# Kernel optimization log

Hardware: AMD Instinct MI355X
Metric: run time of the kernel (lower is better)

## Reference

```python
import jax, jax.numpy as jnp
import numpy as np

TOK = 256        # flattened batch*seq tokens (decode-style, memory-bound)
IN_F = 4096
OUT_F = 4096
N_OUTLIER = 32


def quantize_rowwise(x):
    """Symmetric rowwise int8 quantization: scale = rowwise absmax."""
    scale = jnp.max(jnp.abs(x), axis=-1)                      # [rows]
    safe = jnp.maximum(scale, 1e-8)
    q = jnp.clip(jnp.round(x / safe[:, None] * 127.0), -127.0, 127.0)
    return q, scale


def setup_inputs() -> dict:
    key = jax.random.key(0)
    k1, k2, k3, k4, k5 = jax.random.split(key, 5)
    x = jax.random.normal(k1, (TOK, IN_F), jnp.float32)
    weight_int8 = jax.random.randint(k2, (OUT_F, IN_F), -127, 128, jnp.int32)
    weight_scales = jax.random.uniform(k3, (OUT_F,), jnp.float32, minval=0.5, maxval=2.0)
    # spread unique outlier column indices across in_features
    outlier_indices = jnp.arange(N_OUTLIER, dtype=jnp.int32) * (IN_F // N_OUTLIER)
    outlier_weights = jax.random.normal(k4, (OUT_F, N_OUTLIER), jnp.float32) * 0.02
    bias = jax.random.normal(k5, (OUT_F,), jnp.float32) * 0.01
    # from_linear zeros outlier columns of the int8 weight before quantization
    weight_int8 = weight_int8.at[:, outlier_indices].set(0)
    return {"x": x, "weight_int8": weight_int8, "weight_scales": weight_scales,
            "outlier_indices": outlier_indices, "outlier_weights": outlier_weights,
            "bias": bias}


def reference(x, weight_int8, weight_scales, outlier_indices, outlier_weights, bias):
    # _forward_mixed: outlier columns handled in fp, rest quantize->dequant int8.
    # Selecting the non-outlier columns is equivalent to zeroing the outlier
    # columns (the dropped weight columns contribute 0 to the GEMM, and the
    # rowwise absmax scale is unaffected since |0| = 0). This keeps shapes
    # static and jit-friendly while computing identical math.
    in_f = x.shape[-1]
    mask = jnp.ones((in_f,), dtype=bool).at[outlier_indices].set(False)

    x_main = x * mask                                         # [T, in]
    xq, xs = quantize_rowwise(x_main)                         # int8-valued fp, [T]
    x_fp = xq * (xs[:, None] / 127.0)                         # dequantized activations

    w_fp = (weight_int8 * mask).astype(jnp.float32) * (weight_scales[:, None] / 127.0)  # [out, in]
    out_main = x_fp @ w_fp.T                                  # [T, out]

    x_outlier = x[:, outlier_indices]                         # [T, n_out]
    out_outlier = x_outlier @ outlier_weights.T               # [T, out]

    return out_main + out_outlier + bias
```

## Files before the change

### kernel.cpp

```cpp
#include <hip/hip_runtime.h>
#include <stdint.h>

#define TOK 256
#define IN_F 4096
#define OUT_F 4096
#define N_OUT 32

#define BN 16
#define MACRO_K 512
#define NMACRO (IN_F / MACRO_K)
#define KSTEPS (MACRO_K / 64)

typedef int v4i __attribute__((ext_vector_type(4)));

__global__ __launch_bounds__(256) void oal_quant(
    const float* __restrict__ x, const int* __restrict__ oidx,
    int8_t* __restrict__ xq, float* __restrict__ xs, float* __restrict__ xo)
{
    const int row = blockIdx.x;
    const int tid = threadIdx.x;
    __shared__ unsigned char flags[IN_F];
    __shared__ float wmax[4];
    __shared__ float s_scale;

    *reinterpret_cast<uint4*>(&flags[tid * 16]) = make_uint4(0u, 0u, 0u, 0u);
    __syncthreads();
    if (tid < N_OUT) flags[oidx[tid]] = 1;
    __syncthreads();

    const float* xr = x + (size_t)row * IN_F;
    float4 v[4];
    const float4* xp = reinterpret_cast<const float4*>(xr + tid * 16);
    #pragma unroll
    for (int i = 0; i < 4; ++i) v[i] = xp[i];

    uint4 f = *reinterpret_cast<const uint4*>(&flags[tid * 16]);
    unsigned int fw[4] = { f.x, f.y, f.z, f.w };
    float vals[16];
    #pragma unroll
    for (int i = 0; i < 4; ++i) {
        vals[i*4+0] = ((fw[i]      ) & 255u) ? 0.0f : v[i].x;
        vals[i*4+1] = ((fw[i] >>  8) & 255u) ? 0.0f : v[i].y;
        vals[i*4+2] = ((fw[i] >> 16) & 255u) ? 0.0f : v[i].z;
        vals[i*4+3] = ((fw[i] >> 24) & 255u) ? 0.0f : v[i].w;
    }

    float m = 0.0f;
    #pragma unroll
    for (int i = 0; i < 16; ++i) m = fmaxf(m, fabsf(vals[i]));
    #pragma unroll
    for (int off = 32; off > 0; off >>= 1) m = fmaxf(m, __shfl_xor(m, off, 64));
    const int lane = tid & 63, wid = tid >> 6;
    if (lane == 0) wmax[wid] = m;
    __syncthreads();
    if (tid == 0) {
        float s = fmaxf(fmaxf(wmax[0], wmax[1]), fmaxf(wmax[2], wmax[3]));
        s_scale = s;
        xs[row] = s;
    }
    __syncthreads();
    const float safe = fmaxf(s_scale, 1e-8f);

    int q[16];
    #pragma unroll
    for (int i = 0; i < 16; ++i) {
        float t = vals[i] / safe * 127.0f;
        t = fminf(127.0f, fmaxf(-127.0f, rintf(t)));
        q[i] = (int)t;
    }
    uint4 packed;
    unsigned int* pw = &packed.x;
    #pragma unroll
    for (int i = 0; i < 4; ++i)
        pw[i] = (unsigned)(q[i*4] & 255) | ((unsigned)(q[i*4+1] & 255) << 8)
              | ((unsigned)(q[i*4+2] & 255) << 16) | ((unsigned)(q[i*4+3] & 255) << 24);
    *reinterpret_cast<uint4*>(xq + (size_t)row * IN_F + tid * 16) = packed;

    if (tid < N_OUT) xo[row * N_OUT + tid] = xr[oidx[tid]];
}

__global__ __launch_bounds__(512, 2) void oal_gemm(
    const int8_t* __restrict__ xq, const int* __restrict__ w,
    const float* __restrict__ xs, const float* __restrict__ wscale,
    const float* __restrict__ ow, const float* __restrict__ bias,
    const float* __restrict__ xo, float* __restrict__ out)
{
    const int bn = blockIdx.x;
    const int tid = threadIdx.x;
    const int lane = tid & 63;
    const int wv = tid >> 6;

    __shared__ __align__(16) signed char Bs[2][BN][528];
    __shared__ __align__(16) float XO[TOK][N_OUT];

    {
        const float4* src = reinterpret_cast<const float4*>(xo);
        float4* dst = reinterpret_cast<float4*>(&XO[0][0]);
        #pragma unroll
        for (int i = 0; i < 4; ++i) dst[tid * 4 + i] = src[tid * 4 + i];
    }

    const int sr = tid >> 5;
    const int sc = tid & 31;
    const int* wbase = w + (size_t)(bn * BN + sr) * IN_F + sc * 16;

    int4 wr_[4];
    auto load_regs = [&](int mm) {
        const int4* p = reinterpret_cast<const int4*>(wbase + mm * MACRO_K);
        #pragma unroll
        for (int i = 0; i < 4; ++i) wr_[i] = p[i];
    };
    auto pack_store = [&](int buf) {
        int p[4];
        #pragma unroll
        for (int i = 0; i < 4; ++i) {
            int4 a = wr_[i];
            p[i] = (a.x & 255) | ((a.y & 255) << 8) | ((a.z & 255) << 16) | ((a.w & 255) << 24);
        }
        *reinterpret_cast<int4*>(&Bs[buf][sr][sc * 16]) = make_int4(p[0], p[1], p[2], p[3]);
    };

    const int mrow = wv * 32;
    const int koff_lane = (lane >> 4) * 16;
    const int8_t* a0p = xq + (size_t)(mrow + (lane & 15)) * IN_F + koff_lane;
    const int8_t* a1p = a0p + 16 * IN_F;

    v4i acc0 = {0, 0, 0, 0}, acc1 = {0, 0, 0, 0};

    load_regs(0);
    pack_store(0);
    load_regs(1);
    __syncthreads();

    #pragma unroll
    for (int mm = 0; mm < NMACRO; ++mm) {
        const int cur = mm & 1;
        #pragma unroll
        for (int kk = 0; kk < KSTEPS; ++kk) {
            const int kg = mm * MACRO_K + kk * 64;
            v4i av0 = *reinterpret_cast<const v4i*>(a0p + kg);
            v4i av1 = *reinterpret_cast<const v4i*>(a1p + kg);
            v4i bv  = *reinterpret_cast<const v4i*>(&Bs[cur][lane & 15][kk * 64 + koff_lane]);
            acc0 = __builtin_amdgcn_mfma_i32_16x16x64_i8(av0, bv, acc0, 0, 0, 0);
            acc1 = __builtin_amdgcn_mfma_i32_16x16x64_i8(av1, bv, acc1, 0, 0, 0);
        }
        if (mm < NMACRO - 1) {
            pack_store(cur ^ 1);
            if (mm < NMACRO - 2) load_regs(mm + 2);
            __syncthreads();
        }
    }

    const int ocol = bn * BN + (lane & 15);
    const float wsc = wscale[ocol] * (1.0f / 16129.0f);
    const float bo  = bias[ocol];
    float4 owr[8];
    const float4* owp = reinterpret_cast<const float4*>(ow + (size_t)ocol * N_OUT);
    #pragma unroll
    for (int i = 0; i < 8; ++i) owr[i] = owp[i];

    const int rbase = (lane >> 4) * 4;
    #pragma unroll
    for (int mt = 0; mt < 2; ++mt) {
        v4i a = mt ? acc1 : acc0;
        #pragma unroll
        for (int r = 0; r < 4; ++r) {
            const int t = mrow + mt * 16 + rbase + r;
            const float* xr2 = &XO[t][0];
            float dot = 0.0f;
            #pragma unroll
            for (int j = 0; j < 8; ++j) {
                float4 o4 = owr[j];
                dot += xr2[j*4+0]*o4.x + xr2[j*4+1]*o4.y + xr2[j*4+2]*o4.z + xr2[j*4+3]*o4.w;
            }
            out[(size_t)t * OUT_F + ocol] = (float)a[r] * (xs[t] * wsc) + bo + dot;
        }
    }
}

extern "C" void kernel_launch(void* const* d_in, const int* in_sizes, int n_in,
                              void* d_out, int out_size, void* d_ws, size_t ws_size,
                              hipStream_t stream) {
    const float* x      = (const float*)d_in[0];
    const int*   w      = (const int*)  d_in[1];
    const float* wscale = (const float*)d_in[2];
    const int*   oidx   = (const int*)  d_in[3];
    const float* ow     = (const float*)d_in[4];
    const float* bias   = (const float*)d_in[5];
    float* out = (float*)d_out;

    int8_t* xq = (int8_t*)d_ws;
    float*  xs = (float*)((char*)d_ws + (size_t)TOK * IN_F);
    float*  xo = (float*)((char*)d_ws + (size_t)TOK * IN_F + 1024);

    oal_quant<<<TOK, 256, 0, stream>>>(x, oidx, xq, xs, xo);
    oal_gemm<<<OUT_F / BN, 512, 0, stream>>>(xq, w, xs, wscale, ow, bias, xo, out);
}
```

Baseline: 138.8 us.

## Deepen weight prefetch to two stages and register-pipeline activation loads

The GEMM now keeps two register sets of int32 weights in flight, prefetching macro-tile mm+3 while packing mm+1, so the global-load latency is hidden across more compute. Activation fragments for the MFMA are held in a four-deep register ring and loaded four k-steps ahead instead of just before use. Launch bounds drop from two blocks per SM to one to give the extra registers room, and the quant kernel issues its x loads before the shared-flag setup barriers. The trade is higher register pressure and lower occupancy in exchange for more memory-level parallelism.

```diff
diff --git a/kernel.cpp b/kernel.cpp
--- a/kernel.cpp
+++ b/kernel.cpp
@@ -7,9 +7,10 @@
 #define N_OUT 32
 
 #define BN 16
-#define MACRO_K 512
-#define NMACRO (IN_F / MACRO_K)
-#define KSTEPS (MACRO_K / 64)
+#define KSTEP 64
+#define NK 64
+#define KPM 8
+#define NMACRO 8
 
 typedef int v4i __attribute__((ext_vector_type(4)));
 
@@ -23,16 +24,16 @@
     __shared__ float wmax[4];
     __shared__ float s_scale;
 
-    *reinterpret_cast<uint4*>(&flags[tid * 16]) = make_uint4(0u, 0u, 0u, 0u);
-    __syncthreads();
-    if (tid < N_OUT) flags[oidx[tid]] = 1;
-    __syncthreads();
-
     const float* xr = x + (size_t)row * IN_F;
     float4 v[4];
     const float4* xp = reinterpret_cast<const float4*>(xr + tid * 16);
     #pragma unroll
     for (int i = 0; i < 4; ++i) v[i] = xp[i];
+
+    *reinterpret_cast<uint4*>(&flags[tid * 16]) = make_uint4(0u, 0u, 0u, 0u);
+    __syncthreads();
+    if (tid < N_OUT) flags[oidx[tid]] = 1;
+    __syncthreads();
 
     uint4 f = *reinterpret_cast<const uint4*>(&flags[tid * 16]);
     unsigned int fw[4] = { f.x, f.y, f.z, f.w };
@@ -79,7 +80,7 @@
     if (tid < N_OUT) xo[row * N_OUT + tid] = xr[oidx[tid]];
 }
 
-__global__ __launch_bounds__(512, 2) void oal_gemm(
+__global__ __launch_bounds__(512, 1) void oal_gemm(
     const int8_t* __restrict__ xq, const int* __restrict__ w,
     const float* __restrict__ xs, const float* __restrict__ wscale,
     const float* __restrict__ ow, const float* __restrict__ bias,
@@ -104,52 +105,63 @@
     const int sc = tid & 31;
     const int* wbase = w + (size_t)(bn * BN + sr) * IN_F + sc * 16;
 
-    int4 wr_[4];
-    auto load_regs = [&](int mm) {
-        const int4* p = reinterpret_cast<const int4*>(wbase + mm * MACRO_K);
+    int4 wa[4], wb[4];
+
+#define LOADW(R, mm) { const int4* p_ = reinterpret_cast<const int4*>(wbase + (mm) * (KPM * KSTEP)); \
+    R[0] = p_[0]; R[1] = p_[1]; R[2] = p_[2]; R[3] = p_[3]; }
+
+#define PACKW(R, buf) { int pk0_ = (R[0].x & 255) | ((R[0].y & 255) << 8) | ((R[0].z & 255) << 16) | ((R[0].w & 255) << 24); \
+    int pk1_ = (R[1].x & 255) | ((R[1].y & 255) << 8) | ((R[1].z & 255) << 16) | ((R[1].w & 255) << 24); \
+    int pk2_ = (R[2].x & 255) | ((R[2].y & 255) << 8) | ((R[2].z & 255) << 16) | ((R[2].w & 255) << 24); \
+    int pk3_ = (R[3].x & 255) | ((R[3].y & 255) << 8) | ((R[3].z & 255) << 16) | ((R[3].w & 255) << 24); \
+    *reinterpret_cast<int4*>(&Bs[buf][sr][sc * 16]) = make_int4(pk0_, pk1_, pk2_, pk3_); }
+
+    const int mrow = wv * 32;
+    const int koff = (lane >> 4) * 16;
+    const int8_t* a0p = xq + (size_t)(mrow + (lane & 15)) * IN_F + koff;
+    const int8_t* a1p = a0p + 16 * IN_F;
+
+    v4i acc0 = {0, 0, 0, 0}, acc1 = {0, 0, 0, 0};
+    v4i ar0[4], ar1[4];
+
+    LOADW(wa, 0);
+    LOADW(wb, 1);
+    #pragma unroll
+    for (int i = 0; i < 4; ++i) {
+        ar0[i] = *reinterpret_cast<const v4i*>(a0p + i * KSTEP);
+        ar1[i] = *reinterpret_cast<const v4i*>(a1p + i * KSTEP);
+    }
+    PACKW(wa, 0);
+    LOADW(wa, 2);
+    __syncthreads();
+
+    #pragma unroll
+    for (int mm = 0; mm < NMACRO; ++mm) {
         #pragma unroll
-        for (int i = 0; i < 4; ++i) wr_[i] = p[i];
-    };
-    auto pack_store = [&](int buf) {
-        int p[4];
-        #pragma unroll
-        for (int i = 0; i < 4; ++i) {
-            int4 a = wr_[i];
-            p[i] = (a.x & 255) | ((a.y & 255) << 8) | ((a.z & 255) << 16) | ((a.w & 255) << 24);
-        }
-        *reinterpret_cast<int4*>(&Bs[buf][sr][sc * 16]) = make_int4(p[0], p[1], p[2], p[3]);
-    };
-
-    const int mrow = wv * 32;
-    const int koff_lane = (lane >> 4) * 16;
-    const int8_t* a0p = xq + (size_t)(mrow + (lane & 15)) * IN_F + koff_lane;
-    const int8_t* a1p = a0p + 16 * IN_F;
-
-    v4i acc0 = {0, 0, 0, 0}, acc1 = {0, 0, 0, 0};
-
-    load_regs(0);
-    pack_store(0);
-    load_regs(1);
-    __syncthreads();
-
-    #pragma unroll
-    for (int mm = 0; mm < NMACRO; ++mm) {
-        const int cur = mm & 1;
-        #pragma unroll
-        for (int kk = 0; kk < KSTEPS; ++kk) {
-            const int kg = mm * MACRO_K + kk * 64;
-            v4i av0 = *reinterpret_cast<const v4i*>(a0p + kg);
-            v4i av1 = *reinterpret_cast<const v4i*>(a1p + kg);
-            v4i bv  = *reinterpret_cast<const v4i*>(&Bs[cur][lane & 15][kk * 64 + koff_lane]);
-            acc0 = __builtin_amdgcn_mfma_i32_16x16x64_i8(av0, bv, acc0, 0, 0, 0);
-            acc1 = __builtin_amdgcn_mfma_i32_16x16x64_i8(av1, bv, acc1, 0, 0, 0);
+        for (int kk = 0; kk < KPM; ++kk) {
+            const int ks = mm * KPM + kk;
+            v4i bv = *reinterpret_cast<const v4i*>(&Bs[mm & 1][lane & 15][kk * KSTEP + koff]);
+            acc0 = __builtin_amdgcn_mfma_i32_16x16x64_i8(ar0[ks & 3], bv, acc0, 0, 0, 0);
+            acc1 = __builtin_amdgcn_mfma_i32_16x16x64_i8(ar1[ks & 3], bv, acc1, 0, 0, 0);
+            if (ks + 4 < NK) {
+                ar0[ks & 3] = *reinterpret_cast<const v4i*>(a0p + (ks + 4) * KSTEP);
+                ar1[ks & 3] = *reinterpret_cast<const v4i*>(a1p + (ks + 4) * KSTEP);
+            }
         }
         if (mm < NMACRO - 1) {
-            pack_store(cur ^ 1);
-            if (mm < NMACRO - 2) load_regs(mm + 2);
+            if ((mm & 1) == 0) {
+                PACKW(wb, (mm + 1) & 1);
+                if (mm + 3 < NMACRO) LOADW(wb, mm + 3);
+            } else {
+                PACKW(wa, (mm + 1) & 1);
+                if (mm + 3 < NMACRO) LOADW(wa, mm + 3);
+            }
             __syncthreads();
         }
     }
+
+#undef LOADW
+#undef PACKW
 
     const int ocol = bn * BN + (lane & 15);
     const float wsc = wscale[ocol] * (1.0f / 16129.0f);
```

After: 137.2 us. Within noise of the previous version (-1.1%).

## Stage activations into LDS via async global_load_lds with triple-buffered K pipeline

Applied to the files above, without the earlier changes.

The quant kernel now writes the int8 activations in a K-tiled, XOR-swizzled layout, so each 64-wide K slice of all tokens is contiguous. The GEMM uses global_load_lds to stream those tiles directly into a three-stage LDS ring. Weights are loaded as small per-step chunks and packed into a swizzled LDS buffer, with manual vmcnt/lgkmcnt waits and raw barriers. The outlier activations are now read from global memory instead of being staged in LDS. This aims to cut redundant global activation loads and overlap memory with MFMA, at the cost of a barrier every 64-K step and lower occupancy (launch bounds set to 1 block per CU).

```diff
diff --git a/kernel.cpp b/kernel.cpp
--- a/kernel.cpp
+++ b/kernel.cpp
@@ -5,17 +5,25 @@
 #define IN_F 4096
 #define OUT_F 4096
 #define N_OUT 32
-
 #define BN 16
-#define MACRO_K 512
-#define NMACRO (IN_F / MACRO_K)
-#define KSTEPS (MACRO_K / 64)
+#define TILE_A 16384
 
 typedef int v4i __attribute__((ext_vector_type(4)));
+
+typedef const __attribute__((address_space(1))) void cg_void;
+typedef __attribute__((address_space(3))) void lds_void;
+
+__device__ __forceinline__ void gll16(const void* g, void* l) {
+    __builtin_amdgcn_global_load_lds((cg_void*)g, (lds_void*)l, 16, 0, 0);
+}
+
+#define VMCNT(n) asm volatile("s_waitcnt vmcnt(" #n ")" ::: "memory")
+#define LGKM0()  asm volatile("s_waitcnt lgkmcnt(0)" ::: "memory")
+#define FENCE()  asm volatile("" ::: "memory")
 
 __global__ __launch_bounds__(256) void oal_quant(
     const float* __restrict__ x, const int* __restrict__ oidx,
-    int8_t* __restrict__ xq, float* __restrict__ xs, float* __restrict__ xo)
+    int8_t* __restrict__ xqt, float* __restrict__ xs, float* __restrict__ xo)
 {
     const int row = blockIdx.x;
     const int tid = threadIdx.x;
@@ -23,16 +31,16 @@
     __shared__ float wmax[4];
     __shared__ float s_scale;
 
-    *reinterpret_cast<uint4*>(&flags[tid * 16]) = make_uint4(0u, 0u, 0u, 0u);
-    __syncthreads();
-    if (tid < N_OUT) flags[oidx[tid]] = 1;
-    __syncthreads();
-
     const float* xr = x + (size_t)row * IN_F;
     float4 v[4];
     const float4* xp = reinterpret_cast<const float4*>(xr + tid * 16);
     #pragma unroll
     for (int i = 0; i < 4; ++i) v[i] = xp[i];
+
+    *reinterpret_cast<uint4*>(&flags[tid * 16]) = make_uint4(0u, 0u, 0u, 0u);
+    __syncthreads();
+    if (tid < N_OUT) flags[oidx[tid]] = 1;
+    __syncthreads();
 
     uint4 f = *reinterpret_cast<const uint4*>(&flags[tid * 16]);
     unsigned int fw[4] = { f.x, f.y, f.z, f.w };
@@ -74,82 +82,99 @@
     for (int i = 0; i < 4; ++i)
         pw[i] = (unsigned)(q[i*4] & 255) | ((unsigned)(q[i*4+1] & 255) << 8)
               | ((unsigned)(q[i*4+2] & 255) << 16) | ((unsigned)(q[i*4+3] & 255) << 24);
-    *reinterpret_cast<uint4*>(xq + (size_t)row * IN_F + tid * 16) = packed;
+
+    const int ks = tid >> 2;
+    const int c  = tid & 3;
+    const int sw = c ^ ((row >> 1) & 3);
+    *reinterpret_cast<uint4*>(xqt + (size_t)ks * TILE_A + row * 64 + sw * 16) = packed;
 
     if (tid < N_OUT) xo[row * N_OUT + tid] = xr[oidx[tid]];
 }
 
-__global__ __launch_bounds__(512, 2) void oal_gemm(
-    const int8_t* __restrict__ xq, const int* __restrict__ w,
+__global__ __launch_bounds__(512, 1) void oal_gemm(
+    const int8_t* __restrict__ xqt, const int* __restrict__ wgt,
     const float* __restrict__ xs, const float* __restrict__ wscale,
     const float* __restrict__ ow, const float* __restrict__ bias,
     const float* __restrict__ xo, float* __restrict__ out)
 {
+    __shared__ __align__(16) int8_t As[3][TILE_A];
+    __shared__ __align__(16) int8_t Bp[3][1024];
+
     const int bn = blockIdx.x;
     const int tid = threadIdx.x;
     const int lane = tid & 63;
     const int wv = tid >> 6;
-
-    __shared__ __align__(16) signed char Bs[2][BN][528];
-    __shared__ __align__(16) float XO[TOK][N_OUT];
-
-    {
-        const float4* src = reinterpret_cast<const float4*>(xo);
-        float4* dst = reinterpret_cast<float4*>(&XO[0][0]);
-        #pragma unroll
-        for (int i = 0; i < 4; ++i) dst[tid * 4 + i] = src[tid * 4 + i];
-    }
-
-    const int sr = tid >> 5;
-    const int sc = tid & 31;
-    const int* wbase = w + (size_t)(bn * BN + sr) * IN_F + sc * 16;
-
-    int4 wr_[4];
-    auto load_regs = [&](int mm) {
-        const int4* p = reinterpret_cast<const int4*>(wbase + mm * MACRO_K);
-        #pragma unroll
-        for (int i = 0; i < 4; ++i) wr_[i] = p[i];
-    };
-    auto pack_store = [&](int buf) {
-        int p[4];
-        #pragma unroll
-        for (int i = 0; i < 4; ++i) {
-            int4 a = wr_[i];
-            p[i] = (a.x & 255) | ((a.y & 255) << 8) | ((a.z & 255) << 16) | ((a.w & 255) << 24);
-        }
-        *reinterpret_cast<int4*>(&Bs[buf][sr][sc * 16]) = make_int4(p[0], p[1], p[2], p[3]);
-    };
-
-    const int mrow = wv * 32;
-    const int koff_lane = (lane >> 4) * 16;
-    const int8_t* a0p = xq + (size_t)(mrow + (lane & 15)) * IN_F + koff_lane;
-    const int8_t* a1p = a0p + 16 * IN_F;
-
-    v4i acc0 = {0, 0, 0, 0}, acc1 = {0, 0, 0, 0};
-
-    load_regs(0);
-    pack_store(0);
-    load_regs(1);
-    __syncthreads();
-
-    #pragma unroll
-    for (int mm = 0; mm < NMACRO; ++mm) {
-        const int cur = mm & 1;
-        #pragma unroll
-        for (int kk = 0; kk < KSTEPS; ++kk) {
-            const int kg = mm * MACRO_K + kk * 64;
-            v4i av0 = *reinterpret_cast<const v4i*>(a0p + kg);
-            v4i av1 = *reinterpret_cast<const v4i*>(a1p + kg);
-            v4i bv  = *reinterpret_cast<const v4i*>(&Bs[cur][lane & 15][kk * 64 + koff_lane]);
-            acc0 = __builtin_amdgcn_mfma_i32_16x16x64_i8(av0, bv, acc0, 0, 0, 0);
-            acc1 = __builtin_amdgcn_mfma_i32_16x16x64_i8(av1, bv, acc1, 0, 0, 0);
-        }
-        if (mm < NMACRO - 1) {
-            pack_store(cur ^ 1);
-            if (mm < NMACRO - 2) load_regs(mm + 2);
-            __syncthreads();
-        }
-    }
+    const int kof = lane >> 4;
+
+    const int r0 = wv * 32 + (lane & 15);
+    const int r1 = r0 + 16;
+    const int a0off = r0 * 64 + ((kof ^ ((r0 >> 1) & 3)) * 16);
+    const int a1off = r1 * 64 + ((kof ^ ((r1 >> 1) & 3)) * 16);
+    const int rb = lane & 15;
+    const int boff = rb * 64 + ((kof ^ ((rb >> 1) & 3)) * 16);
+
+    const int8_t* asrc0 = xqt + (size_t)(wv * 64 + lane) * 16;
+    const int8_t* asrc1 = xqt + (size_t)((8 + wv) * 64 + lane) * 16;
+
+    const int brow = tid >> 5;
+    const int bdw  = (2 * tid) & 63;
+    const int* bsrc = wgt + (size_t)(bn * BN + brow) * IN_F + bdw;
+    const int bpoff = brow * 64 + (((bdw >> 4) ^ ((brow >> 1) & 3)) * 16) + (bdw & 15);
+
+    v4i acc0 = {0,0,0,0}, acc1 = {0,0,0,0};
+    uint2 braw0, braw1;
+
+    gll16(asrc0, &As[0][wv * 1024]);
+    gll16(asrc1, &As[0][(8 + wv) * 1024]);
+    braw0 = *reinterpret_cast<const uint2*>(bsrc);
+    asrc0 += TILE_A; asrc1 += TILE_A; bsrc += 64;
+    gll16(asrc0, &As[1][wv * 1024]);
+    gll16(asrc1, &As[1][(8 + wv) * 1024]);
+    braw1 = *reinterpret_cast<const uint2*>(bsrc);
+    asrc0 += TILE_A; asrc1 += TILE_A; bsrc += 64;
+    VMCNT(0);
+    *reinterpret_cast<uint16_t*>(&Bp[0][bpoff]) =
+        (uint16_t)((braw0.x & 255) | ((braw0.y & 255) << 8));
+    LGKM0();
+    __builtin_amdgcn_s_barrier();
+    FENCE();
+
+#define PHASE(SR, SS, SW, BIN, BOUT, STAGE, FINAL, VMN)                          \
+    {                                                                            \
+        if (STAGE) {                                                             \
+            gll16(asrc0, &As[SS][wv * 1024]);                                    \
+            gll16(asrc1, &As[SS][(8 + wv) * 1024]);                              \
+            BIN = *reinterpret_cast<const uint2*>(bsrc);                         \
+            asrc0 += TILE_A; asrc1 += TILE_A; bsrc += 64;                        \
+        }                                                                        \
+        v4i a0_ = *reinterpret_cast<const v4i*>(&As[SR][a0off]);                 \
+        v4i a1_ = *reinterpret_cast<const v4i*>(&As[SR][a1off]);                 \
+        v4i bv_ = *reinterpret_cast<const v4i*>(&Bp[SR][boff]);                  \
+        acc0 = __builtin_amdgcn_mfma_i32_16x16x64_i8(a0_, bv_, acc0, 0, 0, 0);   \
+        acc1 = __builtin_amdgcn_mfma_i32_16x16x64_i8(a1_, bv_, acc1, 0, 0, 0);   \
+        if (!(FINAL)) {                                                          \
+            VMCNT(VMN);                                                          \
+            *reinterpret_cast<uint16_t*>(&Bp[SW][bpoff]) =                       \
+                (uint16_t)((BOUT.x & 255) | ((BOUT.y & 255) << 8));              \
+            LGKM0();                                                             \
+            __builtin_amdgcn_s_barrier();                                        \
+            FENCE();                                                             \
+        }                                                                        \
+    }
+
+    for (int kb = 0; kb < 60; kb += 6) {
+        PHASE(0,2,1, braw0, braw1, 1, 0, 3);
+        PHASE(1,0,2, braw1, braw0, 1, 0, 3);
+        PHASE(2,1,0, braw0, braw1, 1, 0, 3);
+        PHASE(0,2,1, braw1, braw0, 1, 0, 3);
+        PHASE(1,0,2, braw0, braw1, 1, 0, 3);
+        PHASE(2,1,0, braw1, braw0, 1, 0, 3);
+    }
+    PHASE(0,2,1, braw0, braw1, 1, 0, 3);
+    PHASE(1,0,2, braw1, braw0, 1, 0, 3);
+    PHASE(2,0,0, braw0, braw1, 0, 0, 0);
+    PHASE(0,0,0, braw0, braw0, 0, 1, 0);
+#undef PHASE
 
     const int ocol = bn * BN + (lane & 15);
     const float wsc = wscale[ocol] * (1.0f / 16129.0f);
@@ -159,19 +184,21 @@
     #pragma unroll
     for (int i = 0; i < 8; ++i) owr[i] = owp[i];
 
-    const int rbase = (lane >> 4) * 4;
+    const int rbase = kof * 4;
+    const int mrow = wv * 32;
     #pragma unroll
     for (int mt = 0; mt < 2; ++mt) {
         v4i a = mt ? acc1 : acc0;
         #pragma unroll
         for (int r = 0; r < 4; ++r) {
             const int t = mrow + mt * 16 + rbase + r;
-            const float* xr2 = &XO[t][0];
+            const float4* xr4 = reinterpret_cast<const float4*>(xo + (size_t)t * N_OUT);
             float dot = 0.0f;
             #pragma unroll
             for (int j = 0; j < 8; ++j) {
                 float4 o4 = owr[j];
-                dot += xr2[j*4+0]*o4.x + xr2[j*4+1]*o4.y + xr2[j*4+2]*o4.z + xr2[j*4+3]*o4.w;
+                float4 x4 = xr4[j];
+                dot += x4.x*o4.x + x4.y*o4.y + x4.z*o4.z + x4.w*o4.w;
             }
             out[(size_t)t * OUT_F + ocol] = (float)a[r] * (xs[t] * wsc) + bo + dot;
         }
@@ -189,10 +216,10 @@
     const float* bias   = (const float*)d_in[5];
     float* out = (float*)d_out;
 
-    int8_t* xq = (int8_t*)d_ws;
-    float*  xs = (float*)((char*)d_ws + (size_t)TOK * IN_F);
-    float*  xo = (float*)((char*)d_ws + (size_t)TOK * IN_F + 1024);
-
-    oal_quant<<<TOK, 256, 0, stream>>>(x, oidx, xq, xs, xo);
-    oal_gemm<<<OUT_F / BN, 512, 0, stream>>>(xq, w, xs, wscale, ow, bias, xo, out);
-}
+    int8_t* xqt = (int8_t*)d_ws;
+    float*  xs  = (float*)((char*)d_ws + (size_t)TOK * IN_F);
+    float*  xo  = (float*)((char*)d_ws + (size_t)TOK * IN_F + 1024);
+
+    oal_quant<<<TOK, 256, 0, stream>>>(x, oidx, xqt, xs, xo);
+    oal_gemm<<<OUT_F / BN, 512, 0, stream>>>(xqt, w, xs, wscale, ow, bias, xo, out);
+}
```

Result: no change. 138.4 us (-0.3%).

## Preload full weight tile into LDS and software-pipeline A loads with inline asm

Applied to the files above, without the earlier changes.

The GEMM now loads and packs each block's entire 16x4096 int32 weight slice into a 64KB LDS buffer once, laid out k-major, then runs the K loop without intermediate barriers. Activation fragments are streamed with an 8-deep register ring using inline-asm global loads and explicit vmcnt waits, so MFMAs overlap with outstanding global loads. The outlier activation tile is read straight from global memory instead of being staged in LDS. The quant kernel issues its x loads before the flag setup. The larger LDS footprint may reduce occupancy, and the hand-counted waitcnts make correctness depend on the exact number of loads in flight.

```diff
diff --git a/kernel.cpp b/kernel.cpp
--- a/kernel.cpp
+++ b/kernel.cpp
@@ -5,13 +5,14 @@
 #define IN_F 4096
 #define OUT_F 4096
 #define N_OUT 32
-
 #define BN 16
-#define MACRO_K 512
-#define NMACRO (IN_F / MACRO_K)
-#define KSTEPS (MACRO_K / 64)
 
 typedef int v4i __attribute__((ext_vector_type(4)));
+
+#define ALD(D, P, OFF) \
+    asm volatile("global_load_dwordx4 %0, %1, off offset:" OFF \
+                 : "=v"(D) : "v"(P) : "memory")
+#define WAITV(N) asm volatile("s_waitcnt vmcnt(" N ")" ::: "memory")
 
 __global__ __launch_bounds__(256) void oal_quant(
     const float* __restrict__ x, const int* __restrict__ oidx,
@@ -23,16 +24,16 @@
     __shared__ float wmax[4];
     __shared__ float s_scale;
 
-    *reinterpret_cast<uint4*>(&flags[tid * 16]) = make_uint4(0u, 0u, 0u, 0u);
-    __syncthreads();
-    if (tid < N_OUT) flags[oidx[tid]] = 1;
-    __syncthreads();
-
     const float* xr = x + (size_t)row * IN_F;
     float4 v[4];
     const float4* xp = reinterpret_cast<const float4*>(xr + tid * 16);
     #pragma unroll
     for (int i = 0; i < 4; ++i) v[i] = xp[i];
+
+    *reinterpret_cast<uint4*>(&flags[tid * 16]) = make_uint4(0u, 0u, 0u, 0u);
+    __syncthreads();
+    if (tid < N_OUT) flags[oidx[tid]] = 1;
+    __syncthreads();
 
     uint4 f = *reinterpret_cast<const uint4*>(&flags[tid * 16]);
     unsigned int fw[4] = { f.x, f.y, f.z, f.w };
@@ -80,76 +81,92 @@
 }
 
 __global__ __launch_bounds__(512, 2) void oal_gemm(
-    const int8_t* __restrict__ xq, const int* __restrict__ w,
+    const int8_t* __restrict__ xq, const int* __restrict__ wgt,
     const float* __restrict__ xs, const float* __restrict__ wscale,
     const float* __restrict__ ow, const float* __restrict__ bias,
     const float* __restrict__ xo, float* __restrict__ out)
 {
+    __shared__ __align__(16) int8_t Bs[64 * 1024];
+
     const int bn = blockIdx.x;
     const int tid = threadIdx.x;
     const int lane = tid & 63;
     const int wv = tid >> 6;
-
-    __shared__ __align__(16) signed char Bs[2][BN][528];
-    __shared__ __align__(16) float XO[TOK][N_OUT];
+    const int kof = lane >> 4;
 
     {
-        const float4* src = reinterpret_cast<const float4*>(xo);
-        float4* dst = reinterpret_cast<float4*>(&XO[0][0]);
-        #pragma unroll
-        for (int i = 0; i < 4; ++i) dst[tid * 4 + i] = src[tid * 4 + i];
-    }
-
-    const int sr = tid >> 5;
-    const int sc = tid & 31;
-    const int* wbase = w + (size_t)(bn * BN + sr) * IN_F + sc * 16;
-
-    int4 wr_[4];
-    auto load_regs = [&](int mm) {
-        const int4* p = reinterpret_cast<const int4*>(wbase + mm * MACRO_K);
-        #pragma unroll
-        for (int i = 0; i < 4; ++i) wr_[i] = p[i];
-    };
-    auto pack_store = [&](int buf) {
-        int p[4];
-        #pragma unroll
-        for (int i = 0; i < 4; ++i) {
-            int4 a = wr_[i];
-            p[i] = (a.x & 255) | ((a.y & 255) << 8) | ((a.z & 255) << 16) | ((a.w & 255) << 24);
-        }
-        *reinterpret_cast<int4*>(&Bs[buf][sr][sc * 16]) = make_int4(p[0], p[1], p[2], p[3]);
-    };
-
-    const int mrow = wv * 32;
-    const int koff_lane = (lane >> 4) * 16;
-    const int8_t* a0p = xq + (size_t)(mrow + (lane & 15)) * IN_F + koff_lane;
+        const int r = tid >> 5;
+        const int ii = tid & 31;
+        const int* gsrc = wgt + (size_t)(bn * BN + r) * IN_F + ii * 4;
+        const int lbase = (ii >> 4) * 1024 + r * 64 + (ii & 15) * 4;
+
+        auto packw = [](int4 a) -> unsigned {
+            return (unsigned)((a.x & 255) | ((a.y & 255) << 8)
+                            | ((a.z & 255) << 16) | ((a.w & 255) << 24));
+        };
+        int4 sA[8], sB[8];
+        #pragma unroll
+        for (int j = 0; j < 8; ++j) sA[j] = *reinterpret_cast<const int4*>(gsrc + j * 128);
+        #pragma unroll
+        for (int j = 0; j < 8; ++j) sB[j] = *reinterpret_cast<const int4*>(gsrc + (8 + j) * 128);
+        #pragma unroll
+        for (int j = 0; j < 8; ++j) *reinterpret_cast<unsigned*>(&Bs[lbase + j * 2048]) = packw(sA[j]);
+        #pragma unroll
+        for (int j = 0; j < 8; ++j) sA[j] = *reinterpret_cast<const int4*>(gsrc + (16 + j) * 128);
+        #pragma unroll
+        for (int j = 0; j < 8; ++j) *reinterpret_cast<unsigned*>(&Bs[lbase + (8 + j) * 2048]) = packw(sB[j]);
+        #pragma unroll
+        for (int j = 0; j < 8; ++j) sB[j] = *reinterpret_cast<const int4*>(gsrc + (24 + j) * 128);
+        #pragma unroll
+        for (int j = 0; j < 8; ++j) *reinterpret_cast<unsigned*>(&Bs[lbase + (16 + j) * 2048]) = packw(sA[j]);
+        #pragma unroll
+        for (int j = 0; j < 8; ++j) *reinterpret_cast<unsigned*>(&Bs[lbase + (24 + j) * 2048]) = packw(sB[j]);
+    }
+    __syncthreads();
+
+    const int r0 = wv * 32 + (lane & 15);
+    const int8_t* a0p = xq + (size_t)r0 * IN_F + kof * 16;
     const int8_t* a1p = a0p + 16 * IN_F;
-
-    v4i acc0 = {0, 0, 0, 0}, acc1 = {0, 0, 0, 0};
-
-    load_regs(0);
-    pack_store(0);
-    load_regs(1);
-    __syncthreads();
-
-    #pragma unroll
-    for (int mm = 0; mm < NMACRO; ++mm) {
-        const int cur = mm & 1;
-        #pragma unroll
-        for (int kk = 0; kk < KSTEPS; ++kk) {
-            const int kg = mm * MACRO_K + kk * 64;
-            v4i av0 = *reinterpret_cast<const v4i*>(a0p + kg);
-            v4i av1 = *reinterpret_cast<const v4i*>(a1p + kg);
-            v4i bv  = *reinterpret_cast<const v4i*>(&Bs[cur][lane & 15][kk * 64 + koff_lane]);
-            acc0 = __builtin_amdgcn_mfma_i32_16x16x64_i8(av0, bv, acc0, 0, 0, 0);
-            acc1 = __builtin_amdgcn_mfma_i32_16x16x64_i8(av1, bv, acc1, 0, 0, 0);
-        }
-        if (mm < NMACRO - 1) {
-            pack_store(cur ^ 1);
-            if (mm < NMACRO - 2) load_regs(mm + 2);
-            __syncthreads();
-        }
-    }
+    const int8_t* bptr = &Bs[(lane & 15) * 64 + kof * 16];
+
+    v4i ar0[8], ar1[8];
+    v4i acc0 = {0,0,0,0}, acc1 = {0,0,0,0};
+
+    ALD(ar0[0], a0p, "0");   ALD(ar1[0], a1p, "0");
+    ALD(ar0[1], a0p, "64");  ALD(ar1[1], a1p, "64");
+    ALD(ar0[2], a0p, "128"); ALD(ar1[2], a1p, "128");
+    ALD(ar0[3], a0p, "192"); ALD(ar1[3], a1p, "192");
+    ALD(ar0[4], a0p, "256"); ALD(ar1[4], a1p, "256");
+    ALD(ar0[5], a0p, "320"); ALD(ar1[5], a1p, "320");
+    ALD(ar0[6], a0p, "384"); ALD(ar1[6], a1p, "384");
+    ALD(ar0[7], a0p, "448"); ALD(ar1[7], a1p, "448");
+
+#define KS(SLOT, KOFF, ROFF) { \
+    v4i bv_ = *reinterpret_cast<const v4i*>(bptr + (KOFF) * 1024); \
+    WAITV("14"); \
+    __builtin_amdgcn_sched_barrier(0); \
+    acc0 = __builtin_amdgcn_mfma_i32_16x16x64_i8(ar0[SLOT], bv_, acc0, 0, 0, 0); \
+    acc1 = __builtin_amdgcn_mfma_i32_16x16x64_i8(ar1[SLOT], bv_, acc1, 0, 0, 0); \
+    ALD(ar0[SLOT], a0p, ROFF); \
+    ALD(ar1[SLOT], a1p, ROFF); \
+}
+#define KT(SLOT, KOFF, VN) { \
+    v4i bv_ = *reinterpret_cast<const v4i*>(bptr + (KOFF) * 1024); \
+    WAITV(VN); \
+    __builtin_amdgcn_sched_barrier(0); \
+    acc0 = __builtin_amdgcn_mfma_i32_16x16x64_i8(ar0[SLOT], bv_, acc0, 0, 0, 0); \
+    acc1 = __builtin_amdgcn_mfma_i32_16x16x64_i8(ar1[SLOT], bv_, acc1, 0, 0, 0); \
+}
+
+    for (int blk = 0; blk < 7; ++blk) {
+        KS(0, 0, "512"); KS(1, 1, "576"); KS(2, 2, "640"); KS(3, 3, "704");
+        KS(4, 4, "768"); KS(5, 5, "832"); KS(6, 6, "896"); KS(7, 7, "960");
+        a0p += 512; a1p += 512; bptr += 8192;
+    }
+    KT(0, 0, "14"); KT(1, 1, "12"); KT(2, 2, "10"); KT(3, 3, "8");
+    KT(4, 4, "6");  KT(5, 5, "4");  KT(6, 6, "2");  KT(7, 7, "0");
+#undef KS
+#undef KT
 
     const int ocol = bn * BN + (lane & 15);
     const float wsc = wscale[ocol] * (1.0f / 16129.0f);
@@ -159,19 +176,21 @@
     #pragma unroll
     for (int i = 0; i < 8; ++i) owr[i] = owp[i];
 
-    const int rbase = (lane >> 4) * 4;
+    const int rbase = kof * 4;
+    const int mrow = wv * 32;
     #pragma unroll
     for (int mt = 0; mt < 2; ++mt) {
         v4i a = mt ? acc1 : acc0;
         #pragma unroll
         for (int r = 0; r < 4; ++r) {
             const int t = mrow + mt * 16 + rbase + r;
-            const float* xr2 = &XO[t][0];
+            const float4* xr4 = reinterpret_cast<const float4*>(xo + (size_t)t * N_OUT);
             float dot = 0.0f;
             #pragma unroll
             for (int j = 0; j < 8; ++j) {
                 float4 o4 = owr[j];
-                dot += xr2[j*4+0]*o4.x + xr2[j*4+1]*o4.y + xr2[j*4+2]*o4.z + xr2[j*4+3]*o4.w;
+                float4 x4 = xr4[j];
+                dot += x4.x*o4.x + x4.y*o4.y + x4.z*o4.z + x4.w*o4.w;
             }
             out[(size_t)t * OUT_F + ocol] = (float)a[r] * (xs[t] * wsc) + bo + dot;
         }
```

Result: slower. 142.2 us (+2.5%).
